# Kernel tuning notes

Measured on AMD Instinct MI355X. Metric: run time of the kernel, lower is better.

Reference implementation:

```python
import jax, jax.numpy as jnp
import numpy as np
from jax import lax

B, N, F_IN, T = 1024, 22, 32, 32
K = 3
CHEV = 64     # nb_chev_filter
TIMEF = 64    # nb_time_filter
LN_EPS = 1e-5


def setup_inputs() -> dict:
    key = jax.random.key(0)
    ks = jax.random.split(key, 19)
    rn = lambda k, shape, s=0.1: (jax.random.normal(k, shape, jnp.float32) * s)
    return {
        "x": rn(ks[0], (B, N, F_IN, T), 1.0),
        # Temporal_Attention_layer params
        "U1": rn(ks[1], (N,)),
        "U2": rn(ks[2], (F_IN, N)),
        "U3": rn(ks[3], (F_IN,)),
        "be": rn(ks[4], (1, T, T)),
        "Ve": rn(ks[5], (T, T)),
        # Spatial_Attention_layer params
        "W1": rn(ks[6], (T,)),
        "W2": rn(ks[7], (F_IN, T)),
        "W3": rn(ks[8], (F_IN,)),
        "bs": rn(ks[9], (1, N, N)),
        "Vs": rn(ks[10], (N, N)),
        # cheb_conv_withSAt params
        "Theta": rn(ks[11], (K, F_IN, CHEV)),
        "node_emb": rn(ks[12], (N, N), 1.0),
        # time conv (1x3, pad (0,1)) and residual conv (1x1)
        "tconv_w": rn(ks[13], (TIMEF, CHEV, 1, 3)),
        "tconv_b": rn(ks[14], (TIMEF,)),
        "rconv_w": rn(ks[15], (TIMEF, F_IN, 1, 1)),
        "rconv_b": rn(ks[16], (TIMEF,)),
        # LayerNorm over nb_time_filter
        "ln_g": jnp.ones((TIMEF,), jnp.float32),
        "ln_b": jnp.zeros((TIMEF,), jnp.float32),
    }


def reference(x, U1, U2, U3, be, Ve, W1, W2, W3, bs, Vs, Theta, node_emb,
              tconv_w, tconv_b, rconv_w, rconv_b, ln_g, ln_b):
    Bx, Nx, Fx, Tx = x.shape

    # ---- Temporal attention: E_normalized [B, T, T] ----
    # lhs = ((x.permute(0,3,2,1) @ U1) @ U2)  -> [B, T, N]
    lhs_t = jnp.einsum('bnft,n->btf', x, U1) @ U2          # [B,T,N]
    rhs_t = jnp.einsum('f,bnft->bnt', U3, x)               # [B,N,T]
    prod_t = jnp.einsum('btn,bns->bts', lhs_t, rhs_t)      # [B,T,T]
    E = jnp.einsum('ts,bsu->btu', Ve, jax.nn.sigmoid(prod_t + be))
    E_norm = jax.nn.softmax(E, axis=1)                     # softmax over dim=1

    # x_TAt = reshape(x, [B, N*F, T]) @ E_norm  -> [B, N, F, T]
    x_TAt = (x.reshape(Bx, Nx * Fx, Tx) @ E_norm).reshape(Bx, Nx, Fx, Tx)

    # ---- Spatial attention on x_TAt: S_normalized [B, N, N] ----
    lhs_s = jnp.einsum('bnft,t->bnf', x_TAt, W1) @ W2      # [B,N,T]
    rhs_s = jnp.einsum('f,bnft->bnt', W3, x_TAt)           # [B,N,T]
    prod_s = jnp.einsum('bnt,bmt->bnm', lhs_s, rhs_s)      # [B,N,N]
    S = jnp.einsum('nm,bml->bnl', Vs, jax.nn.sigmoid(prod_s + bs))
    S_norm = jax.nn.softmax(S, axis=1)                     # softmax over dim=1

    # ---- Chebyshev graph conv with adaptive supports (vectorized over T) ----
    supports = jax.nn.softmax(jax.nn.relu(node_emb @ node_emb.T), axis=1)
    support_set = [jnp.eye(Nx, dtype=x.dtype), supports]
    for _ in range(2, K):
        support_set.append(2.0 * supports @ support_set[-1] - support_set[-2])

    out = jnp.zeros((Bx, Nx, CHEV, Tx), x.dtype)
    for k in range(K):
        A_k = support_set[k][None, :, :] * S_norm          # [B,N,N]
        # rhs[b,m,f,t] = sum_n A_k[b,n,m] * x[b,n,f,t]  (A_k^T @ graph_signal)
        rhs = jnp.einsum('bnm,bnft->bmft', A_k, x)
        out = out + jnp.einsum('bmft,fo->bmot', rhs, Theta[k])
    spatial_gcn = jax.nn.relu(out)                         # [B,N,CHEV,T]

    # ---- Temporal conv (1x3, pad (0,1)) on [B, CHEV, N, T] ----
    dn = ('NCHW', 'OIHW', 'NCHW')
    t_in = spatial_gcn.transpose(0, 2, 1, 3)               # [B,CHEV,N,T]
    t_out = lax.conv_general_dilated(t_in, tconv_w, (1, 1), ((0, 0), (1, 1)),
                                     dimension_numbers=dn)
    t_out = t_out + tconv_b[None, :, None, None]           # [B,TIMEF,N,T]

    # ---- Residual conv (1x1) on [B, F_in, N, T] ----
    r_in = x.transpose(0, 2, 1, 3)
    r_out = lax.conv_general_dilated(r_in, rconv_w, (1, 1), ((0, 0), (0, 0)),
                                     dimension_numbers=dn)
    r_out = r_out + rconv_b[None, :, None, None]           # [B,TIMEF,N,T]

    # ---- Residual add, ReLU, LayerNorm over channel dim ----
    y = jax.nn.relu(r_out + t_out).transpose(0, 3, 2, 1)   # [B,T,N,TIMEF]
    mu = jnp.mean(y, axis=-1, keepdims=True)
    var = jnp.var(y, axis=-1, keepdims=True)
    y = (y - mu) * lax.rsqrt(var + LN_EPS) * ln_g + ln_b
    return y.transpose(0, 2, 3, 1)                         # [B,N,TIMEF,T]
```

## Files before the change

kernel.cpp:

```cpp
#include <hip/hip_runtime.h>
#include <hip/hip_bf16.h>
#include <math.h>


typedef unsigned short u16;
typedef __attribute__((ext_vector_type(8))) short short8;
typedef __attribute__((ext_vector_type(4))) float f32x4;
typedef __attribute__((ext_vector_type(2))) float f32x2;

__device__ __forceinline__ float sigm(float v){ return 1.f/(1.f+expf(-v)); }

__device__ __forceinline__ u16 f2bf(float x){
  __hip_bfloat16 h = __float2bfloat16(x);
  return *reinterpret_cast<u16*>(&h);
}
__device__ __forceinline__ unsigned f2bf2(float lo, float hi){
  return (unsigned)f2bf(lo) | ((unsigned)f2bf(hi) << 16);
}

__global__ void k_sup_prep(const float* __restrict__ emb, float* __restrict__ wsT,
                           const float* __restrict__ Theta,
                           const float* __restrict__ tw, const float* __restrict__ tb,
                           const float* __restrict__ rw, const float* __restrict__ rb,
                           u16* __restrict__ thA, u16* __restrict__ wA, float* __restrict__ wsB){
  if (blockIdx.x < 81){
    int tid = blockIdx.x*256 + threadIdx.x;
    if (tid < 6144){
      int j = tid&7, l = (tid>>3)&63, blk = tid>>9;
      int ks = blk>>2, ci = blk&3, r = l&15, g = l>>4;
      int kf = 32*ks + 8*g + j, c = 16*ci + r;
      thA[tid] = f2bf(Theta[kf*64 + c]);
    } else if (tid < 20480){
      int e = tid - 6144;
      int j = e&7, l = (e>>3)&63, blk = e>>9;
      int ks = blk>>2, oi = blk&3, r = l&15, g = l>>4;
      int k = 32*ks + 8*g + j, o = 16*oi + r;
      float v = (k < 192) ? tw[o*192 + (k&63)*3 + (k>>6)] : rw[o*32 + (k-192)];
      wA[e] = f2bf(v);
    } else if (tid < 20544){
      int o = tid - 20480; wsB[o] = tb[o] + rb[o];
    }
    return;
  }
  __shared__ float M[484];
  __shared__ float T1s[484];
  int tid = threadIdx.x;
  for (int idx=tid; idx<484; idx+=256){
    int n = idx/22, m = idx - (idx/22)*22;
    float s = 0.f;
    for (int j=0;j<22;j++) s += emb[n*22+j]*emb[m*22+j];
    M[idx] = fmaxf(s, 0.f);
  }
  __syncthreads();
  if (tid < 22){
    float mx = -1e30f;
    for (int m=0;m<22;m++) mx = fmaxf(mx, M[tid*22+m]);
    float s = 0.f;
    for (int m=0;m<22;m++) s += expf(M[tid*22+m]-mx);
    float inv = 1.f/s;
    for (int m=0;m<22;m++) T1s[tid*22+m] = expf(M[tid*22+m]-mx)*inv;
  }
  __syncthreads();
  for (int idx=tid; idx<484; idx+=256){
    int n = idx/22, m = idx - (idx/22)*22;
    float s = 0.f;
    for (int p=0;p<22;p++) s += T1s[n*22+p]*T1s[p*22+m];
    wsT[idx]      = T1s[idx];
    wsT[484+idx]  = 2.f*s - ((n==m)?1.f:0.f);
  }
}

__global__ __launch_bounds__(512) void k_attn(
    const float* __restrict__ x,
    const float* __restrict__ U1, const float* __restrict__ U2, const float* __restrict__ U3,
    const float* __restrict__ be, const float* __restrict__ Ve,
    const float* __restrict__ W1, const float* __restrict__ W2, const float* __restrict__ W3,
    const float* __restrict__ bs, const float* __restrict__ Vs,
    float* __restrict__ snorm){
  int b = blockIdx.x, tid = threadIdx.x;
  const float* xb = x + (size_t)b*22528;
  __shared__ float xu1[1024];
  __shared__ float rhs_t[704];
  __shared__ float lhs_t[704];
  __shared__ float sigp[1024];
  __shared__ float Em[1024];
  __shared__ float sm[1024];
  __shared__ float w1e[32];
  __shared__ float xw3[704];
  __shared__ float lhsS[704];
  __shared__ float lhs2[704];
  __shared__ float rhsS[704];
  __shared__ float sig2[484];
  __shared__ float Sl[484];

  for (int idx=tid; idx<1024; idx+=512){
    float a=0.f;
    for (int n=0;n<22;n++) a = fmaf(xb[n*1024 + idx], U1[n], a);
    xu1[idx]=a;
  }
  for (int idx=tid; idx<704; idx+=512){
    int n = idx>>5, t = idx&31; float a=0.f, c=0.f;
    for (int f=0;f<32;f++){ float xv = xb[n*1024+f*32+t]; a = fmaf(U3[f],xv,a); c = fmaf(W3[f],xv,c); }
    rhs_t[idx]=a; xw3[idx]=c;
  }
  __syncthreads();
  for (int idx=tid; idx<704; idx+=512){
    int t = idx/22, n2 = idx - t*22; float a=0.f;
    for (int f=0;f<32;f++) a = fmaf(xu1[f*32+t], U2[f*22+n2], a);
    lhs_t[idx]=a;
  }
  __syncthreads();
  for (int idx=tid; idx<1024; idx+=512){
    int s = idx>>5, u = idx&31; float p=0.f;
    for (int n=0;n<22;n++) p = fmaf(lhs_t[s*22+n], rhs_t[n*32+u], p);
    sigp[idx] = sigm(p + be[idx]);
  }
  __syncthreads();
  for (int idx=tid; idx<1024; idx+=512){
    int t = idx>>5, u = idx&31; float a=0.f;
    for (int s2=0;s2<32;s2++) a = fmaf(Ve[t*32+s2], sigp[s2*32+u], a);
    Em[idx]=a;
  }
  __syncthreads();
  {
    int u = tid>>4, th = tid&15;
    float e0 = Em[(2*th)*32 + u], e1 = Em[(2*th+1)*32 + u];
    float mx = fmaxf(e0, e1);
    #pragma unroll
    for (int mask=1; mask<16; mask<<=1) mx = fmaxf(mx, __shfl_xor(mx, mask));
    float x0 = expf(e0-mx), x1 = expf(e1-mx);
    float s = x0 + x1;
    #pragma unroll
    for (int mask=1; mask<16; mask<<=1) s += __shfl_xor(s, mask);
    float inv = 1.f/s;
    sm[(2*th)*32 + u]   = x0*inv;
    sm[(2*th+1)*32 + u] = x1*inv;
  }
  __syncthreads();
  {
    int u = tid>>4, th = tid&15;
    float pw = fmaf(sm[u*32 + 2*th], W1[2*th], sm[u*32 + 2*th+1]*W1[2*th+1]);
    #pragma unroll
    for (int mask=1; mask<16; mask<<=1) pw += __shfl_xor(pw, mask);
    if (th==0) w1e[u] = pw;
  }
  __syncthreads();
  for (int idx=tid; idx<704; idx+=512){
    int n = idx>>5, f = idx&31; float a=0.f;
    for (int u=0;u<32;u++) a = fmaf(xb[n*1024+f*32+u], w1e[u], a);
    lhsS[idx]=a;
  }
  __syncthreads();
  for (int idx=tid; idx<704; idx+=512){
    int n = idx>>5, t = idx&31; float a=0.f;
    for (int f=0;f<32;f++) a = fmaf(lhsS[n*32+f], W2[f*32+t], a);
    lhs2[idx]=a;
  }
  for (int idx=tid; idx<704; idx+=512){
    int mm = idx>>5, t = idx&31; float a=0.f;
    for (int u=0;u<32;u++) a = fmaf(xw3[mm*32+u], sm[u*32+t], a);
    rhsS[idx]=a;
  }
  __syncthreads();
  for (int idx=tid; idx<484; idx+=512){
    int a_ = idx/22, l = idx - (idx/22)*22; float p=0.f;
    for (int t=0;t<32;t++) p = fmaf(lhs2[a_*32+t], rhsS[l*32+t], p);
    sig2[idx] = sigm(p + bs[idx]);
  }
  __syncthreads();
  for (int idx=tid; idx<484; idx+=512){
    int n = idx/22, l = idx - (idx/22)*22; float s=0.f;
    for (int mm=0;mm<22;mm++) s = fmaf(Vs[n*22+mm], sig2[mm*22+l], s);
    Sl[idx]=s;
  }
  __syncthreads();
  {
    int grp = tid>>5, nn = tid&31;
    for (int l = grp; l < 22; l += 16){
      float v = (nn<22) ? Sl[nn*22 + l] : -1e30f;
      float mx = v;
      #pragma unroll
      for (int mask=1; mask<32; mask<<=1) mx = fmaxf(mx, __shfl_xor(mx, mask));
      float e = (nn<22) ? expf(v-mx) : 0.f;
      float s = e;
      #pragma unroll
      for (int mask=1; mask<32; mask<<=1) s += __shfl_xor(s, mask);
      if (nn<22) snorm[(size_t)b*484 + nn*22 + l] = e*(1.f/s);
    }
  }
}

__global__ __launch_bounds__(256, 6) void k_fused(
    const float* __restrict__ x,
    const float* __restrict__ wsT, const float* __restrict__ snorm,
    const u16* __restrict__ thA, const u16* __restrict__ wA, const float* __restrict__ wsB,
    const float* __restrict__ lng, const float* __restrict__ lnb,
    float* __restrict__ out){
  __shared__ __align__(16) u16 GtU[2][32*72];
  __shared__ __align__(16) u16 sgTU[2][34*72];
  __shared__ __align__(16) u16 xTU[2][32*40];
  __shared__ __align__(16) float ak4[22*4];
  __shared__ float smm[2];

  int wg = blockIdx.x;
  int logical = (wg & 7)*1408 + (wg >> 3);
  int b = logical/11, mp = logical - b*11;
  int m0 = mp*2;
  int tid = threadIdx.x;
  const float* xb = x + (size_t)b*22528;

  if (tid < 128){
    int mi = tid>>6, r6 = tid&63;
    int row = (r6>>5) ? 33 : 0, c2 = r6&31;
    *(unsigned*)&sgTU[mi][row*72 + c2*2] = 0u;
  }
  if (tid < 88){
    int n = tid>>2, j = tid&3;
    int mi = j>>1, k1 = j&1;
    int m = m0 + mi;
    ak4[tid] = wsT[k1*484 + n*22 + m] * snorm[(size_t)b*484 + n*22 + m];
  }
  if (tid < 2) smm[tid] = snorm[(size_t)b*484 + (m0+tid)*23];
  __syncthreads();

  {
    f32x2 acc[2][2][2];
    #pragma unroll
    for (int a=0;a<2;a++)
      #pragma unroll
      for (int k1=0;k1<2;k1++){ acc[a][k1][0]=f32x2{0,0}; acc[a][k1][1]=f32x2{0,0}; }
    const float4* x4 = (const float4*)xb;
    #pragma unroll 2
    for (int n=0;n<22;n++){
      float4 av = *(const float4*)&ak4[n*4];
      float4 xv = x4[n*256 + tid];
      f32x2 xlo = {xv.x, xv.y}, xhi = {xv.z, xv.w};
      f32x2 a00 = {av.x, av.x}, a01 = {av.y, av.y};
      f32x2 a10 = {av.z, av.z}, a11 = {av.w, av.w};
      acc[0][0][0] = __builtin_elementwise_fma(a00, xlo, acc[0][0][0]);
      acc[0][0][1] = __builtin_elementwise_fma(a00, xhi, acc[0][0][1]);
      acc[0][1][0] = __builtin_elementwise_fma(a01, xlo, acc[0][1][0]);
      acc[0][1][1] = __builtin_elementwise_fma(a01, xhi, acc[0][1][1]);
      acc[1][0][0] = __builtin_elementwise_fma(a10, xlo, acc[1][0][0]);
      acc[1][0][1] = __builtin_elementwise_fma(a10, xhi, acc[1][0][1]);
      acc[1][1][0] = __builtin_elementwise_fma(a11, xlo, acc[1][1][0]);
      acc[1][1][1] = __builtin_elementwise_fma(a11, xhi, acc[1][1][1]);
    }
    int f = tid>>3, t7 = tid&7, t0 = t7*4;
    int w4 = f>>3, f_low = f&7;
    int gcol0 = 8*((0*4 + w4) ^ t7) + f_low;
    int gcol1 = 8*((1*4 + w4) ^ t7) + f_low;
    int xcol  = 8*(w4 ^ (t7&3)) + f_low;
    #pragma unroll
    for (int mi=0;mi<2;mi++){
      float4 xm = ((const float4*)xb)[(m0+mi)*256 + tid];
      u16* xd = &xTU[mi][0];
      xd[(t0+0)*40 + xcol] = f2bf(xm.x);
      xd[(t0+1)*40 + xcol] = f2bf(xm.y);
      xd[(t0+2)*40 + xcol] = f2bf(xm.z);
      xd[(t0+3)*40 + xcol] = f2bf(xm.w);
      #pragma unroll
      for (int k1=0;k1<2;k1++){
        int gc = k1 ? gcol1 : gcol0;
        u16* gd = &GtU[mi][gc];
        gd[(t0+0)*72] = f2bf(acc[mi][k1][0][0]);
        gd[(t0+1)*72] = f2bf(acc[mi][k1][0][1]);
        gd[(t0+2)*72] = f2bf(acc[mi][k1][1][0]);
        gd[(t0+3)*72] = f2bf(acc[mi][k1][1][1]);
      }
    }
  }
  __syncthreads();

  int w = tid>>6, l = tid&63, r = l&15, g = l>>4;

  {
    const u16* tA = thA + (size_t)(w*64 + l)*8;
    short8 a0 = *(const short8*)(tA);
    short8 a1 = *(const short8*)(tA + 2048);
    short8 a2 = *(const short8*)(tA + 4096);
    #pragma unroll
    for (int mi=0;mi<2;mi++){
      float sm_ = smm[mi];
      #pragma unroll
      for (int ti=0; ti<2; ++ti){
        int row = ti*16 + r;
        int h  = (row>>2)&7;
        int h2 = (row>>2)&3;
        f32x4 a12 = {0.f,0.f,0.f,0.f}, ax = {0.f,0.f,0.f,0.f};
        const u16* gp0 = &GtU[mi][row*72 + 8*((0*4+g)^h)];
        const u16* gp1 = &GtU[mi][row*72 + 8*((1*4+g)^h)];
        a12 = __builtin_amdgcn_mfma_f32_16x16x32_bf16(a1, *(const short8*)(gp0), a12, 0,0,0);
        a12 = __builtin_amdgcn_mfma_f32_16x16x32_bf16(a2, *(const short8*)(gp1), a12, 0,0,0);
        const u16* xp = &xTU[mi][row*40 + 8*(g^h2)];
        ax  = __builtin_amdgcn_mfma_f32_16x16x32_bf16(a0, *(const short8*)(xp),  ax,  0,0,0);
        int orow = 1 + row, c0 = w*16 + g*4;
        float v0 = fmaxf(fmaf(sm_, ax[0], a12[0]), 0.f);
        float v1 = fmaxf(fmaf(sm_, ax[1], a12[1]), 0.f);
        float v2 = fmaxf(fmaf(sm_, ax[2], a12[2]), 0.f);
        float v3 = fmaxf(fmaf(sm_, ax[3], a12[3]), 0.f);
        *(unsigned*)&sgTU[mi][orow*72 + c0]     = f2bf2(v0, v1);
        *(unsigned*)&sgTU[mi][orow*72 + c0 + 2] = f2bf2(v2, v3);
      }
    }
  }
  __syncthreads();

  f32x4 acc[2][2];
  acc[0][0]=f32x4{0,0,0,0}; acc[0][1]=f32x4{0,0,0,0};
  acc[1][0]=f32x4{0,0,0,0}; acc[1][1]=f32x4{0,0,0,0};
  {
    const u16* pA = wA + (size_t)(w*64 + l)*8;
    #pragma unroll
    for (int ks=0; ks<6; ++ks){
      short8 wk = *(const short8*)(pA + ks*2048);
      int seg = ks>>1, colb = (ks&1)*32 + 8*g;
      #pragma unroll
      for (int mi=0;mi<2;mi++){
        const u16* q0 = &sgTU[mi][(r + seg)*72 + colb];
        acc[mi][0] = __builtin_amdgcn_mfma_f32_16x16x32_bf16(wk, *(const short8*)(q0),         acc[mi][0], 0,0,0);
        acc[mi][1] = __builtin_amdgcn_mfma_f32_16x16x32_bf16(wk, *(const short8*)(q0 + 16*72), acc[mi][1], 0,0,0);
      }
    }
    short8 wk = *(const short8*)(pA + 6*2048);
    int h2 = (r>>2)&3;
    #pragma unroll
    for (int mi=0;mi<2;mi++){
      const u16* q = &xTU[mi][r*40 + 8*(g^h2)];
      acc[mi][0] = __builtin_amdgcn_mfma_f32_16x16x32_bf16(wk, *(const short8*)(q),         acc[mi][0], 0,0,0);
      acc[mi][1] = __builtin_amdgcn_mfma_f32_16x16x32_bf16(wk, *(const short8*)(q + 16*40), acc[mi][1], 0,0,0);
    }
  }

  float4 bias4 = ((const float4*)wsB)[w*4 + g];
  float bb[4] = {bias4.x, bias4.y, bias4.z, bias4.w};
  float y[2][2][4];
  float s1[2][2] = {{0.f,0.f},{0.f,0.f}}, s2[2][2] = {{0.f,0.f},{0.f,0.f}};
  #pragma unroll
  for (int mi=0;mi<2;mi++){
    #pragma unroll
    for (int h=0;h<2;h++){
      #pragma unroll
      for (int i=0;i<4;i++){
        float v = fmaxf(acc[mi][h][i] + bb[i], 0.f);
        y[mi][h][i] = v;
        s1[mi][h] += v;
        s2[mi][h] = fmaf(v, v, s2[mi][h]);
      }
      s1[mi][h] += __shfl_xor(s1[mi][h],16); s1[mi][h] += __shfl_xor(s1[mi][h],32);
      s2[mi][h] += __shfl_xor(s2[mi][h],16); s2[mi][h] += __shfl_xor(s2[mi][h],32);
    }
  }
  float* p1 = (float*)&GtU[0][0];
  float* p2 = p1 + 256;
  if (l < 16){
    #pragma unroll
    for (int mi=0;mi<2;mi++){
      p1[(mi*32 + l)*4 + w]      = s1[mi][0];
      p1[(mi*32 + 16 + l)*4 + w] = s1[mi][1];
      p2[(mi*32 + l)*4 + w]      = s2[mi][0];
      p2[(mi*32 + 16 + l)*4 + w] = s2[mi][1];
    }
  }
  __syncthreads();
  float4 g4 = ((const float4*)lng)[w*4 + g];
  float4 b4 = ((const float4*)lnb)[w*4 + g];
  float gg[4]={g4.x,g4.y,g4.z,g4.w}, bgg[4]={b4.x,b4.y,b4.z,b4.w};
  #pragma unroll
  for (int mi=0;mi<2;mi++){
    float4 q1a = ((const float4*)p1)[mi*32 + r],      q2a = ((const float4*)p2)[mi*32 + r];
    float4 q1b = ((const float4*)p1)[mi*32 + 16 + r], q2b = ((const float4*)p2)[mi*32 + 16 + r];
    float S1a = q1a.x+q1a.y+q1a.z+q1a.w, S2a = q2a.x+q2a.y+q2a.z+q2a.w;
    float S1b = q1b.x+q1b.y+q1b.z+q1b.w, S2b = q2b.x+q2b.y+q2b.z+q2b.w;
    float mu0 = S1a*(1.f/64.f), var0 = S2a*(1.f/64.f) - mu0*mu0, rs0 = rsqrtf(var0 + 1e-5f);
    float mu1 = S1b*(1.f/64.f), var1 = S2b*(1.f/64.f) - mu1*mu1, rs1 = rsqrtf(var1 + 1e-5f);
    float* ob = out + ((size_t)(b*22 + m0 + mi)*64 + (w*16 + g*4))*32;
    #pragma unroll
    for (int i=0;i<4;i++){
      ob[i*32 + r]      = (y[mi][0][i]-mu0)*rs0*gg[i] + bgg[i];
      ob[i*32 + 16 + r] = (y[mi][1][i]-mu1)*rs1*gg[i] + bgg[i];
    }
  }
}

extern "C" void kernel_launch(void* const* d_in, const int* in_sizes, int n_in,
                              void* d_out, int out_size, void* d_ws, size_t ws_size,
                              hipStream_t stream){
  const float* x     = (const float*)d_in[0];
  const float* U1    = (const float*)d_in[1];
  const float* U2    = (const float*)d_in[2];
  const float* U3    = (const float*)d_in[3];
  const float* be    = (const float*)d_in[4];
  const float* Ve    = (const float*)d_in[5];
  const float* W1    = (const float*)d_in[6];
  const float* W2    = (const float*)d_in[7];
  const float* W3    = (const float*)d_in[8];
  const float* bs    = (const float*)d_in[9];
  const float* Vs    = (const float*)d_in[10];
  const float* Theta = (const float*)d_in[11];
  const float* emb   = (const float*)d_in[12];
  const float* tw    = (const float*)d_in[13];
  const float* tb    = (const float*)d_in[14];
  const float* rw    = (const float*)d_in[15];
  const float* rb    = (const float*)d_in[16];
  const float* lng   = (const float*)d_in[17];
  const float* lnb   = (const float*)d_in[18];
  float* out = (float*)d_out;
  float* wsf = (float*)d_ws;
  float* wsT   = wsf;
  float* snorm = wsf + 1024;
  u16*   thA   = (u16*)(wsf + 496640);
  u16*   wA    = (u16*)(wsf + 499712);
  float* wsB   = wsf + 506880;

  k_sup_prep<<<82, 256, 0, stream>>>(emb, wsT, Theta, tw, tb, rw, rb, thA, wA, wsB);
  k_attn<<<1024, 512, 0, stream>>>(x, U1,U2,U3, be,Ve, W1,W2,W3, bs,Vs, snorm);
  k_fused<<<1024*11, 256, 0, stream>>>(x, wsT, snorm, thA, wA, wsB, lng, lnb, out);
}
```

Baseline: 152.1 us.

## Make fused kernel loop over all node pairs per batch with hoisted weights

```diff
diff --git a/kernel.cpp b/kernel.cpp
--- a/kernel.cpp
+++ b/kernel.cpp
@@ -190,7 +190,7 @@
   }
 }
 
-__global__ __launch_bounds__(256, 6) void k_fused(
+__global__ __launch_bounds__(256, 4) void k_fused(
     const float* __restrict__ x,
     const float* __restrict__ wsT, const float* __restrict__ snorm,
     const u16* __restrict__ thA, const u16* __restrict__ wA, const float* __restrict__ wsB,
@@ -203,182 +203,186 @@
   __shared__ float smm[2];
 
   int wg = blockIdx.x;
-  int logical = (wg & 7)*1408 + (wg >> 3);
-  int b = logical/11, mp = logical - b*11;
-  int m0 = mp*2;
+  int b = (wg & 7)*128 + (wg >> 3);
   int tid = threadIdx.x;
   const float* xb = x + (size_t)b*22528;
+  const float* snb = snorm + (size_t)b*484;
+
+  int w = tid>>6, l = tid&63, r = l&15, g = l>>4;
+
+  const u16* tA = thA + (size_t)(w*64 + l)*8;
+  short8 a0 = *(const short8*)(tA);
+  short8 a1 = *(const short8*)(tA + 2048);
+  short8 a2 = *(const short8*)(tA + 4096);
+  const u16* pA = wA + (size_t)(w*64 + l)*8;
+  short8 wk7[7];
+  #pragma unroll
+  for (int ks=0; ks<7; ++ks) wk7[ks] = *(const short8*)(pA + ks*2048);
+  float4 bias4 = ((const float4*)wsB)[w*4 + g];
+  float bb[4] = {bias4.x, bias4.y, bias4.z, bias4.w};
+  float4 g4 = ((const float4*)lng)[w*4 + g];
+  float4 b4 = ((const float4*)lnb)[w*4 + g];
+  float gg[4]={g4.x,g4.y,g4.z,g4.w}, bgg[4]={b4.x,b4.y,b4.z,b4.w};
+
+  int fA = tid>>3, t7 = tid&7, t0 = t7*4;
+  int w4 = fA>>3, f_low = fA&7;
+  int gcol0 = 8*((0*4 + w4) ^ t7) + f_low;
+  int gcol1 = 8*((1*4 + w4) ^ t7) + f_low;
+  int xcol  = 8*(w4 ^ (t7&3)) + f_low;
 
   if (tid < 128){
     int mi = tid>>6, r6 = tid&63;
     int row = (r6>>5) ? 33 : 0, c2 = r6&31;
     *(unsigned*)&sgTU[mi][row*72 + c2*2] = 0u;
   }
-  if (tid < 88){
-    int n = tid>>2, j = tid&3;
-    int mi = j>>1, k1 = j&1;
-    int m = m0 + mi;
-    ak4[tid] = wsT[k1*484 + n*22 + m] * snorm[(size_t)b*484 + n*22 + m];
-  }
-  if (tid < 2) smm[tid] = snorm[(size_t)b*484 + (m0+tid)*23];
-  __syncthreads();
-
-  {
-    f32x2 acc[2][2][2];
-    #pragma unroll
-    for (int a=0;a<2;a++)
-      #pragma unroll
-      for (int k1=0;k1<2;k1++){ acc[a][k1][0]=f32x2{0,0}; acc[a][k1][1]=f32x2{0,0}; }
-    const float4* x4 = (const float4*)xb;
-    #pragma unroll 2
-    for (int n=0;n<22;n++){
-      float4 av = *(const float4*)&ak4[n*4];
-      float4 xv = x4[n*256 + tid];
-      f32x2 xlo = {xv.x, xv.y}, xhi = {xv.z, xv.w};
-      f32x2 a00 = {av.x, av.x}, a01 = {av.y, av.y};
-      f32x2 a10 = {av.z, av.z}, a11 = {av.w, av.w};
-      acc[0][0][0] = __builtin_elementwise_fma(a00, xlo, acc[0][0][0]);
-      acc[0][0][1] = __builtin_elementwise_fma(a00, xhi, acc[0][0][1]);
-      acc[0][1][0] = __builtin_elementwise_fma(a01, xlo, acc[0][1][0]);
-      acc[0][1][1] = __builtin_elementwise_fma(a01, xhi, acc[0][1][1]);
-      acc[1][0][0] = __builtin_elementwise_fma(a10, xlo, acc[1][0][0]);
-      acc[1][0][1] = __builtin_elementwise_fma(a10, xhi, acc[1][0][1]);
-      acc[1][1][0] = __builtin_elementwise_fma(a11, xlo, acc[1][1][0]);
-      acc[1][1][1] = __builtin_elementwise_fma(a11, xhi, acc[1][1][1]);
-    }
-    int f = tid>>3, t7 = tid&7, t0 = t7*4;
-    int w4 = f>>3, f_low = f&7;
-    int gcol0 = 8*((0*4 + w4) ^ t7) + f_low;
-    int gcol1 = 8*((1*4 + w4) ^ t7) + f_low;
-    int xcol  = 8*(w4 ^ (t7&3)) + f_low;
+
+  for (int mp=0; mp<11; ++mp){
+    int m0 = mp*2;
+    if (tid < 88){
+      int n = tid>>2, j = tid&3;
+      int mi = j>>1, k1 = j&1;
+      int m = m0 + mi;
+      ak4[tid] = wsT[k1*484 + n*22 + m] * snb[n*22 + m];
+    }
+    if (tid < 2) smm[tid] = snb[(m0+tid)*23];
+    __syncthreads();
+
+    {
+      f32x2 acc[4][2];
+      #pragma unroll
+      for (int j=0;j<4;j++){ acc[j][0]=f32x2{0,0}; acc[j][1]=f32x2{0,0}; }
+      const float4* x4 = (const float4*)xb;
+      #pragma unroll 2
+      for (int n=0;n<22;n++){
+        float4 av = *(const float4*)&ak4[n*4];
+        float4 xv = x4[n*256 + tid];
+        f32x2 xlo = {xv.x, xv.y}, xhi2 = {xv.z, xv.w};
+        f32x2 c0 = {av.x,av.x}, c1 = {av.y,av.y}, c2 = {av.z,av.z}, c3 = {av.w,av.w};
+        acc[0][0] = __builtin_elementwise_fma(c0, xlo,  acc[0][0]);
+        acc[0][1] = __builtin_elementwise_fma(c0, xhi2, acc[0][1]);
+        acc[1][0] = __builtin_elementwise_fma(c1, xlo,  acc[1][0]);
+        acc[1][1] = __builtin_elementwise_fma(c1, xhi2, acc[1][1]);
+        acc[2][0] = __builtin_elementwise_fma(c2, xlo,  acc[2][0]);
+        acc[2][1] = __builtin_elementwise_fma(c2, xhi2, acc[2][1]);
+        acc[3][0] = __builtin_elementwise_fma(c3, xlo,  acc[3][0]);
+        acc[3][1] = __builtin_elementwise_fma(c3, xhi2, acc[3][1]);
+      }
+      #pragma unroll
+      for (int mi=0;mi<2;mi++){
+        float4 xm = ((const float4*)xb)[(m0+mi)*256 + tid];
+        u16* xd = &xTU[mi][0];
+        xd[(t0+0)*40 + xcol] = f2bf(xm.x);
+        xd[(t0+1)*40 + xcol] = f2bf(xm.y);
+        xd[(t0+2)*40 + xcol] = f2bf(xm.z);
+        xd[(t0+3)*40 + xcol] = f2bf(xm.w);
+        #pragma unroll
+        for (int k1=0;k1<2;k1++){
+          int j = mi*2 + k1;
+          int gc = k1 ? gcol1 : gcol0;
+          u16* gd = &GtU[mi][gc];
+          gd[(t0+0)*72] = f2bf(acc[j][0][0]);
+          gd[(t0+1)*72] = f2bf(acc[j][0][1]);
+          gd[(t0+2)*72] = f2bf(acc[j][1][0]);
+          gd[(t0+3)*72] = f2bf(acc[j][1][1]);
+        }
+      }
+    }
+    __syncthreads();
+
+    {
+      #pragma unroll
+      for (int mi=0;mi<2;mi++){
+        float sm_ = smm[mi];
+        #pragma unroll
+        for (int ti=0; ti<2; ++ti){
+          int row = ti*16 + r;
+          int h  = (row>>2)&7;
+          int h2 = (row>>2)&3;
+          f32x4 a12 = {0.f,0.f,0.f,0.f}, ax = {0.f,0.f,0.f,0.f};
+          const u16* gp0 = &GtU[mi][row*72 + 8*((0*4+g)^h)];
+          const u16* gp1 = &GtU[mi][row*72 + 8*((1*4+g)^h)];
+          a12 = __builtin_amdgcn_mfma_f32_16x16x32_bf16(a1, *(const short8*)(gp0), a12, 0,0,0);
+          a12 = __builtin_amdgcn_mfma_f32_16x16x32_bf16(a2, *(const short8*)(gp1), a12, 0,0,0);
+          const u16* xp = &xTU[mi][row*40 + 8*(g^h2)];
+          ax  = __builtin_amdgcn_mfma_f32_16x16x32_bf16(a0, *(const short8*)(xp),  ax,  0,0,0);
+          int orow = 1 + row, c0 = w*16 + g*4;
+          float v0 = fmaxf(fmaf(sm_, ax[0], a12[0]), 0.f);
+          float v1 = fmaxf(fmaf(sm_, ax[1], a12[1]), 0.f);
+          float v2 = fmaxf(fmaf(sm_, ax[2], a12[2]), 0.f);
+          float v3 = fmaxf(fmaf(sm_, ax[3], a12[3]), 0.f);
+          *(unsigned*)&sgTU[mi][orow*72 + c0]     = f2bf2(v0, v1);
+          *(unsigned*)&sgTU[mi][orow*72 + c0 + 2] = f2bf2(v2, v3);
+        }
+      }
+    }
+    __syncthreads();
+
+    f32x4 acc[2][2];
+    acc[0][0]=f32x4{0,0,0,0}; acc[0][1]=f32x4{0,0,0,0};
+    acc[1][0]=f32x4{0,0,0,0}; acc[1][1]=f32x4{0,0,0,0};
+    {
+      #pragma unroll
+      for (int ks=0; ks<6; ++ks){
+        int seg = ks>>1, colb = (ks&1)*32 + 8*g;
+        #pragma unroll
+        for (int mi=0;mi<2;mi++){
+          const u16* q0 = &sgTU[mi][(r + seg)*72 + colb];
+          acc[mi][0] = __builtin_amdgcn_mfma_f32_16x16x32_bf16(wk7[ks], *(const short8*)(q0),         acc[mi][0], 0,0,0);
+          acc[mi][1] = __builtin_amdgcn_mfma_f32_16x16x32_bf16(wk7[ks], *(const short8*)(q0 + 16*72), acc[mi][1], 0,0,0);
+        }
+      }
+      int h2 = (r>>2)&3;
+      #pragma unroll
+      for (int mi=0;mi<2;mi++){
+        const u16* q = &xTU[mi][r*40 + 8*(g^h2)];
+        acc[mi][0] = __builtin_amdgcn_mfma_f32_16x16x32_bf16(wk7[6], *(const short8*)(q),         acc[mi][0], 0,0,0);
+        acc[mi][1] = __builtin_amdgcn_mfma_f32_16x16x32_bf16(wk7[6], *(const short8*)(q + 16*40), acc[mi][1], 0,0,0);
+      }
+    }
+
+    float y[2][2][4];
+    float s1[2][2] = {{0.f,0.f},{0.f,0.f}}, s2[2][2] = {{0.f,0.f},{0.f,0.f}};
     #pragma unroll
     for (int mi=0;mi<2;mi++){
-      float4 xm = ((const float4*)xb)[(m0+mi)*256 + tid];
-      u16* xd = &xTU[mi][0];
-      xd[(t0+0)*40 + xcol] = f2bf(xm.x);
-      xd[(t0+1)*40 + xcol] = f2bf(xm.y);
-      xd[(t0+2)*40 + xcol] = f2bf(xm.z);
-      xd[(t0+3)*40 + xcol] = f2bf(xm.w);
-      #pragma unroll
-      for (int k1=0;k1<2;k1++){
-        int gc = k1 ? gcol1 : gcol0;
-        u16* gd = &GtU[mi][gc];
-        gd[(t0+0)*72] = f2bf(acc[mi][k1][0][0]);
-        gd[(t0+1)*72] = f2bf(acc[mi][k1][0][1]);
-        gd[(t0+2)*72] = f2bf(acc[mi][k1][1][0]);
-        gd[(t0+3)*72] = f2bf(acc[mi][k1][1][1]);
-      }
-    }
-  }
-  __syncthreads();
-
-  int w = tid>>6, l = tid&63, r = l&15, g = l>>4;
-
-  {
-    const u16* tA = thA + (size_t)(w*64 + l)*8;
-    short8 a0 = *(const short8*)(tA);
-    short8 a1 = *(const short8*)(tA + 2048);
-    short8 a2 = *(const short8*)(tA + 4096);
+      #pragma unroll
+      for (int h=0;h<2;h++){
+        #pragma unroll
+        for (int i=0;i<4;i++){
+          float v = fmaxf(acc[mi][h][i] + bb[i], 0.f);
+          y[mi][h][i] = v;
+          s1[mi][h] += v;
+          s2[mi][h] = fmaf(v, v, s2[mi][h]);
+        }
+        s1[mi][h] += __shfl_xor(s1[mi][h],16); s1[mi][h] += __shfl_xor(s1[mi][h],32);
+        s2[mi][h] += __shfl_xor(s2[mi][h],16); s2[mi][h] += __shfl_xor(s2[mi][h],32);
+      }
+    }
+    float* p1 = (float*)&GtU[0][0];
+    float* p2 = p1 + 256;
+    if (l < 16){
+      #pragma unroll
+      for (int mi=0;mi<2;mi++){
+        p1[(mi*32 + l)*4 + w]      = s1[mi][0];
+        p1[(mi*32 + 16 + l)*4 + w] = s1[mi][1];
+        p2[(mi*32 + l)*4 + w]      = s2[mi][0];
+        p2[(mi*32 + 16 + l)*4 + w] = s2[mi][1];
+      }
+    }
+    __syncthreads();
     #pragma unroll
     for (int mi=0;mi<2;mi++){
-      float sm_ = smm[mi];
-      #pragma unroll
-      for (int ti=0; ti<2; ++ti){
-        int row = ti*16 + r;
-        int h  = (row>>2)&7;
-        int h2 = (row>>2)&3;
-        f32x4 a12 = {0.f,0.f,0.f,0.f}, ax = {0.f,0.f,0.f,0.f};
-        const u16* gp0 = &GtU[mi][row*72 + 8*((0*4+g)^h)];
-        const u16* gp1 = &GtU[mi][row*72 + 8*((1*4+g)^h)];
-        a12 = __builtin_amdgcn_mfma_f32_16x16x32_bf16(a1, *(const short8*)(gp0), a12, 0,0,0);
-        a12 = __builtin_amdgcn_mfma_f32_16x16x32_bf16(a2, *(const short8*)(gp1), a12, 0,0,0);
-        const u16* xp = &xTU[mi][row*40 + 8*(g^h2)];
-        ax  = __builtin_amdgcn_mfma_f32_16x16x32_bf16(a0, *(const short8*)(xp),  ax,  0,0,0);
-        int orow = 1 + row, c0 = w*16 + g*4;
-        float v0 = fmaxf(fmaf(sm_, ax[0], a12[0]), 0.f);
-        float v1 = fmaxf(fmaf(sm_, ax[1], a12[1]), 0.f);
-        float v2 = fmaxf(fmaf(sm_, ax[2], a12[2]), 0.f);
-        float v3 = fmaxf(fmaf(sm_, ax[3], a12[3]), 0.f);
-        *(unsigned*)&sgTU[mi][orow*72 + c0]     = f2bf2(v0, v1);
-        *(unsigned*)&sgTU[mi][orow*72 + c0 + 2] = f2bf2(v2, v3);
-      }
-    }
-  }
-  __syncthreads();
-
-  f32x4 acc[2][2];
-  acc[0][0]=f32x4{0,0,0,0}; acc[0][1]=f32x4{0,0,0,0};
-  acc[1][0]=f32x4{0,0,0,0}; acc[1][1]=f32x4{0,0,0,0};
-  {
-    const u16* pA = wA + (size_t)(w*64 + l)*8;
-    #pragma unroll
-    for (int ks=0; ks<6; ++ks){
-      short8 wk = *(const short8*)(pA + ks*2048);
-      int seg = ks>>1, colb = (ks&1)*32 + 8*g;
-      #pragma unroll
-      for (int mi=0;mi<2;mi++){
-        const u16* q0 = &sgTU[mi][(r + seg)*72 + colb];
-        acc[mi][0] = __builtin_amdgcn_mfma_f32_16x16x32_bf16(wk, *(const short8*)(q0),         acc[mi][0], 0,0,0);
-        acc[mi][1] = __builtin_amdgcn_mfma_f32_16x16x32_bf16(wk, *(const short8*)(q0 + 16*72), acc[mi][1], 0,0,0);
-      }
-    }
-    short8 wk = *(const short8*)(pA + 6*2048);
-    int h2 = (r>>2)&3;
-    #pragma unroll
-    for (int mi=0;mi<2;mi++){
-      const u16* q = &xTU[mi][r*40 + 8*(g^h2)];
-      acc[mi][0] = __builtin_amdgcn_mfma_f32_16x16x32_bf16(wk, *(const short8*)(q),         acc[mi][0], 0,0,0);
-      acc[mi][1] = __builtin_amdgcn_mfma_f32_16x16x32_bf16(wk, *(const short8*)(q + 16*40), acc[mi][1], 0,0,0);
-    }
-  }
-
-  float4 bias4 = ((const float4*)wsB)[w*4 + g];
-  float bb[4] = {bias4.x, bias4.y, bias4.z, bias4.w};
-  float y[2][2][4];
-  float s1[2][2] = {{0.f,0.f},{0.f,0.f}}, s2[2][2] = {{0.f,0.f},{0.f,0.f}};
-  #pragma unroll
-  for (int mi=0;mi<2;mi++){
-    #pragma unroll
-    for (int h=0;h<2;h++){
+      float4 q1a = ((const float4*)p1)[mi*32 + r],      q2a = ((const float4*)p2)[mi*32 + r];
+      float4 q1b = ((const float4*)p1)[mi*32 + 16 + r], q2b = ((const float4*)p2)[mi*32 + 16 + r];
+      float S1a = q1a.x+q1a.y+q1a.z+q1a.w, S2a = q2a.x+q2a.y+q2a.z+q2a.w;
+      float S1b = q1b.x+q1b.y+q1b.z+q1b.w, S2b = q2b.x+q2b.y+q2b.z+q2b.w;
+      float mu0 = S1a*(1.f/64.f), var0 = S2a*(1.f/64.f) - mu0*mu0, rs0 = rsqrtf(var0 + 1e-5f);
+      float mu1 = S1b*(1.f/64.f), var1 = S2b*(1.f/64.f) - mu1*mu1, rs1 = rsqrtf(var1 + 1e-5f);
+      float* ob = out + ((size_t)(b*22 + m0 + mi)*64 + (w*16 + g*4))*32;
       #pragma unroll
       for (int i=0;i<4;i++){
-        float v = fmaxf(acc[mi][h][i] + bb[i], 0.f);
-        y[mi][h][i] = v;
-        s1[mi][h] += v;
-        s2[mi][h] = fmaf(v, v, s2[mi][h]);
-      }
-      s1[mi][h] += __shfl_xor(s1[mi][h],16); s1[mi][h] += __shfl_xor(s1[mi][h],32);
-      s2[mi][h] += __shfl_xor(s2[mi][h],16); s2[mi][h] += __shfl_xor(s2[mi][h],32);
-    }
-  }
-  float* p1 = (float*)&GtU[0][0];
-  float* p2 = p1 + 256;
-  if (l < 16){
-    #pragma unroll
-    for (int mi=0;mi<2;mi++){
-      p1[(mi*32 + l)*4 + w]      = s1[mi][0];
-      p1[(mi*32 + 16 + l)*4 + w] = s1[mi][1];
-      p2[(mi*32 + l)*4 + w]      = s2[mi][0];
-      p2[(mi*32 + 16 + l)*4 + w] = s2[mi][1];
-    }
-  }
-  __syncthreads();
-  float4 g4 = ((const float4*)lng)[w*4 + g];
-  float4 b4 = ((const float4*)lnb)[w*4 + g];
-  float gg[4]={g4.x,g4.y,g4.z,g4.w}, bgg[4]={b4.x,b4.y,b4.z,b4.w};
-  #pragma unroll
-  for (int mi=0;mi<2;mi++){
-    float4 q1a = ((const float4*)p1)[mi*32 + r],      q2a = ((const float4*)p2)[mi*32 + r];
-    float4 q1b = ((const float4*)p1)[mi*32 + 16 + r], q2b = ((const float4*)p2)[mi*32 + 16 + r];
-    float S1a = q1a.x+q1a.y+q1a.z+q1a.w, S2a = q2a.x+q2a.y+q2a.z+q2a.w;
-    float S1b = q1b.x+q1b.y+q1b.z+q1b.w, S2b = q2b.x+q2b.y+q2b.z+q2b.w;
-    float mu0 = S1a*(1.f/64.f), var0 = S2a*(1.f/64.f) - mu0*mu0, rs0 = rsqrtf(var0 + 1e-5f);
-    float mu1 = S1b*(1.f/64.f), var1 = S2b*(1.f/64.f) - mu1*mu1, rs1 = rsqrtf(var1 + 1e-5f);
-    float* ob = out + ((size_t)(b*22 + m0 + mi)*64 + (w*16 + g*4))*32;
-    #pragma unroll
-    for (int i=0;i<4;i++){
-      ob[i*32 + r]      = (y[mi][0][i]-mu0)*rs0*gg[i] + bgg[i];
-      ob[i*32 + 16 + r] = (y[mi][1][i]-mu1)*rs1*gg[i] + bgg[i];
+        ob[i*32 + r]      = (y[mi][0][i]-mu0)*rs0*gg[i] + bgg[i];
+        ob[i*32 + 16 + r] = (y[mi][1][i]-mu1)*rs1*gg[i] + bgg[i];
+      }
     }
   }
 }
@@ -415,5 +419,5 @@
 
   k_sup_prep<<<82, 256, 0, stream>>>(emb, wsT, Theta, tw, tb, rw, rb, thA, wA, wsB);
   k_attn<<<1024, 512, 0, stream>>>(x, U1,U2,U3, be,Ve, W1,W2,W3, bs,Vs, snorm);
-  k_fused<<<1024*11, 256, 0, stream>>>(x, wsT, snorm, thA, wA, wsB, lng, lnb, out);
-}
+  k_fused<<<1024, 256, 0, stream>>>(x, wsT, snorm, thA, wA, wsB, lng, lnb, out);
+}
```

Measured after the change: 238.6 us. +56.9%, slower.
